# Kernel optimization log

Measured on AMD Instinct MI355X. Metric: run time of the kernel, lower is better.

## Reference

```python
import jax, jax.numpy as jnp
import numpy as np

PI = np.pi


def _rot(axis, a):
    c, s = jnp.cos(a), jnp.sin(a)
    o, z = jnp.ones_like(a), jnp.zeros_like(a)
    if axis == 'X':
        flat = (o, z, z, z, c, -s, z, s, c)
    elif axis == 'Y':
        flat = (c, z, s, z, o, z, -s, z, c)
    else:  # 'Z'
        flat = (c, -s, z, s, c, z, z, z, o)
    return jnp.stack(flat, -1).reshape(3, 3)


def setup_inputs() -> dict:
    key = jax.random.key(0)
    k1, k2 = jax.random.split(key)
    H, W = 1080, 1920
    # world points: spread ~50 around origin, camera at z=100 looking back
    PntCld = jax.random.normal(k1, (400000, 3), dtype=jnp.float32) * 50.0
    # detected corners in pixel coordinates
    dtcCor = jax.random.uniform(k2, (128, 2), dtype=jnp.float32) * jnp.array([W, H], jnp.float32)
    cam_pos = jnp.array([0.0, 0.0, 100.0], jnp.float32)
    theta = jnp.array([5.0, -3.0, 10.0], jnp.float32)  # degrees
    view_angle = jnp.array([60.0], jnp.float32)        # degrees
    return {"PntCld": PntCld, "dtcCor": dtcCor, "cam_pos": cam_pos,
            "theta": theta, "view_angle": view_angle, "height": H, "width": W}


def reference(PntCld, dtcCor, cam_pos, theta, view_angle, height, width):
    th = theta * (PI / 180.0)
    R = _rot('Z', th[2]) @ (_rot('Y', th[1]) @ _rot('X', th[0]))  # (3,3)
    f = -height / (2.0 * jnp.tan(view_angle[0] / 2.0 * (PI / 180.0)))
    K = jnp.stack([f, 0.0, width / 2 - 0.5,
                   0.0, f, height / 2 - 0.5,
                   0.0, 0.0, 1.0]).reshape(3, 3)
    translated = PntCld - cam_pos                 # (N_p,3)
    xyz = translated @ R.T                        # rotate each point
    xyz_prime = xyz / xyz[:, 2:3]                 # perspective divide
    uv = xyz_prime @ K.T                          # (N_p,3) pixel coords
    # y-invert and shift by image height, keep (u,v)
    uv_final = jnp.stack([uv[:, 0], height - uv[:, 1]], -1)  # (N_p,2)
    # pairwise squared distances via ||a||^2 + ||b||^2 - 2 a.b (no (N_d,N_p,2) tensor)
    d2 = (jnp.sum(dtcCor ** 2, -1)[:, None]
          + jnp.sum(uv_final ** 2, -1)[None, :]
          - 2.0 * dtcCor @ uv_final.T)            # (N_d,N_p)
    return jnp.sum(jnp.min(d2, axis=1))
```

## Files before the change

kernel.cpp:

```cpp
#include <hip/hip_runtime.h>
#include <math.h>

#define TILE  512
#define BLOCK 256
#define NC    128


__global__ void init_kernel(const float* __restrict__ theta,
                            const float* __restrict__ vang,
                            const int* __restrict__ hh,
                            const int* __restrict__ ww,
                            float* __restrict__ scal,
                            float* __restrict__ out) {
    if (threadIdx.x == 0) {
        const double D2R = 0.017453292519943295;
        double a = (double)theta[0] * D2R;
        double b = (double)theta[1] * D2R;
        double c = (double)theta[2] * D2R;
        double sa = sin(a), ca = cos(a);
        double sb = sin(b), cb = cos(b);
        double sc = sin(c), cc = cos(c);
        double H = (double)hh[0], W = (double)ww[0];
        double fd = -H / (2.0 * tan((double)vang[0] * 0.5 * D2R));
        scal[0] = (float)(cc * cb);
        scal[1] = (float)(cc * sb * sa - sc * ca);
        scal[2] = (float)(cc * sb * ca + sc * sa);
        scal[3] = (float)(sc * cb);
        scal[4] = (float)(sc * sb * sa + cc * ca);
        scal[5] = (float)(sc * sb * ca - cc * sa);
        scal[6] = (float)(-sb);
        scal[7] = (float)(cb * sa);
        scal[8] = (float)(cb * ca);
        scal[9]  = (float)fd;
        scal[10] = (float)(W * 0.5 - 0.5);
        scal[11] = (float)(H * 0.5 + 0.5);
        out[0] = 0.0f;
    }
}

__global__ __launch_bounds__(BLOCK) void proj_min_kernel(
        const float* __restrict__ pnt,
        const float* __restrict__ cor,
        const float* __restrict__ cam,
        const float* __restrict__ scal,
        float* __restrict__ pbmin,
        int n, int NB) {
    __shared__ float4 uvb[TILE];
    __shared__ float red[4 * NC];

    const int tid = threadIdx.x;
    const float r00 = scal[0], r01 = scal[1], r02 = scal[2];
    const float r10 = scal[3], r11 = scal[4], r12 = scal[5];
    const float r20 = scal[6], r21 = scal[7], r22 = scal[8];
    const float f = scal[9], cx = scal[10], cyv = scal[11];
    const float c0 = cam[0], c1 = cam[1], c2 = cam[2];

    const int base = blockIdx.x * TILE;

    #pragma unroll
    for (int k = 0; k < TILE; k += BLOCK) {
        int i = base + k + tid;
        float u = 0.f, vf = 0.f, b2 = 3.0e38f;
        if (i < n) {
            float px = pnt[3 * i], py = pnt[3 * i + 1], pz = pnt[3 * i + 2];
            float tx = px - c0, ty = py - c1, tz = pz - c2;
            float x = fmaf(r00, tx, fmaf(r01, ty, r02 * tz));
            float y = fmaf(r10, tx, fmaf(r11, ty, r12 * tz));
            float z = fmaf(r20, tx, fmaf(r21, ty, r22 * tz));
            float xz = x / z, yz = y / z;
            u  = fmaf(f, xz, cx);
            vf = fmaf(-f, yz, cyv);
            b2 = fmaf(u, u, vf * vf);
        }
        uvb[k + tid] = make_float4(u, vf, b2, 0.f);
    }
    __syncthreads();

    const int lane = tid & 63;
    const int w    = tid >> 6;
    const int h    = lane >> 5;
    const int sl   = lane & 31;
    const int cb   = sl << 2;

    float bx[4], by[4], m[4];
    #pragma unroll
    for (int k = 0; k < 4; ++k) {
        bx[k] = -2.f * cor[2 * (cb + k)];
        by[k] = -2.f * cor[2 * (cb + k) + 1];
        m[k]  = 3.4e38f;
    }

    const float4* p = &uvb[(w << 7) + (h << 6)];
    #pragma unroll 8
    for (int j = 0; j < 64; ++j) {
        float4 q = p[j];
        #pragma unroll
        for (int k = 0; k < 4; ++k)
            m[k] = fminf(m[k], fmaf(bx[k], q.x, fmaf(by[k], q.y, q.z)));
    }

    #pragma unroll
    for (int k = 0; k < 4; ++k)
        m[k] = fminf(m[k], __shfl_xor(m[k], 32));
    if (lane < 32) {
        #pragma unroll
        for (int k = 0; k < 4; ++k)
            red[w * NC + cb + k] = m[k];
    }
    __syncthreads();

    if (tid < NC) {
        float mm = fminf(fminf(red[tid], red[NC + tid]),
                         fminf(red[2 * NC + tid], red[3 * NC + tid]));
        pbmin[tid * NB + blockIdx.x] = mm;
    }
}

__global__ void reduce_kernel(const float* __restrict__ pbmin,
                              const float* __restrict__ cor,
                              float* __restrict__ out, int NB) {
    const int c = blockIdx.x;
    const int t = threadIdx.x;
    const float* row = pbmin + c * NB;
    float m = 3.4e38f;
    for (int i = t; i < NB; i += 64) m = fminf(m, row[i]);
    #pragma unroll
    for (int off = 32; off > 0; off >>= 1)
        m = fminf(m, __shfl_down(m, off));
    if (t == 0) {
        float ax = cor[2 * c], ay = cor[2 * c + 1];
        atomicAdd(out, m + fmaf(ax, ax, ay * ay));
    }
}

extern "C" void kernel_launch(void* const* d_in, const int* in_sizes, int n_in,
                              void* d_out, int out_size, void* d_ws, size_t ws_size,
                              hipStream_t stream) {
    const float* pnt   = (const float*)d_in[0];
    const float* cor   = (const float*)d_in[1];
    const float* cam   = (const float*)d_in[2];
    const float* theta = (const float*)d_in[3];
    const float* vang  = (const float*)d_in[4];
    const int*   hh    = (const int*)d_in[5];
    const int*   ww    = (const int*)d_in[6];

    int n  = in_sizes[0] / 3;
    int NB = (n + TILE - 1) / TILE;

    float* scal  = (float*)d_ws;
    float* pbmin = (float*)((char*)d_ws + 256);

    init_kernel<<<1, 64, 0, stream>>>(theta, vang, hh, ww, scal, (float*)d_out);
    proj_min_kernel<<<NB, BLOCK, 0, stream>>>(pnt, cor, cam, scal, pbmin, n, NB);
    reduce_kernel<<<NC, 64, 0, stream>>>(pbmin, cor, (float*)d_out, NB);
}
```

Measured before the change: 80.52 us.

## Fold init into projection kernel, vectorize point loads, transpose partial-min layout

The separate init kernel is removed. Each block now computes the rotation and intrinsics scalars in thread 0 and shares them through LDS, which trades one launch for redundant per-block double-precision trig. Each thread loads two consecutive points with three float2 loads instead of strided scalar loads. The partial-min buffer is stored block-major so the column reduction reads coalesced-ish across blocks. The atomicAdd is replaced by a staged deterministic double-precision sum kernel, which adds one extra small launch.

```diff
diff --git a/kernel.cpp b/kernel.cpp
--- a/kernel.cpp
+++ b/kernel.cpp
@@ -6,73 +6,92 @@
 #define NC    128
 
 
-__global__ void init_kernel(const float* __restrict__ theta,
-                            const float* __restrict__ vang,
-                            const int* __restrict__ hh,
-                            const int* __restrict__ ww,
-                            float* __restrict__ scal,
-                            float* __restrict__ out) {
-    if (threadIdx.x == 0) {
+__global__ __launch_bounds__(BLOCK) void proj_min_kernel(
+        const float* __restrict__ pnt,
+        const float* __restrict__ cor,
+        const float* __restrict__ cam,
+        const float* __restrict__ theta,
+        const float* __restrict__ vang,
+        const int* __restrict__ hh,
+        const int* __restrict__ ww,
+        float* __restrict__ pbmin,
+        int n) {
+    __shared__ float4 uvb[TILE];
+    __shared__ float red[4 * NC];
+    __shared__ float sc[12];
+
+    const int tid  = threadIdx.x;
+    const int base = blockIdx.x * TILE;
+
+    const int i0 = base + 2 * tid;
+    float p0x = 0.f, p0y = 0.f, p0z = 0.f;
+    float p1x = 0.f, p1y = 0.f, p1z = 0.f;
+    const bool v0 = (i0 < n), v1 = (i0 + 1 < n);
+    if (v1) {
+        const float2* q = (const float2*)(pnt + 3 * i0);
+        float2 a = q[0], b = q[1], c = q[2];
+        p0x = a.x; p0y = a.y; p0z = b.x;
+        p1x = b.y; p1y = c.x; p1z = c.y;
+    } else if (v0) {
+        p0x = pnt[3 * i0]; p0y = pnt[3 * i0 + 1]; p0z = pnt[3 * i0 + 2];
+    }
+
+    if (tid == 0) {
         const double D2R = 0.017453292519943295;
         double a = (double)theta[0] * D2R;
         double b = (double)theta[1] * D2R;
         double c = (double)theta[2] * D2R;
         double sa = sin(a), ca = cos(a);
         double sb = sin(b), cb = cos(b);
-        double sc = sin(c), cc = cos(c);
+        double sc_ = sin(c), cc = cos(c);
         double H = (double)hh[0], W = (double)ww[0];
         double fd = -H / (2.0 * tan((double)vang[0] * 0.5 * D2R));
-        scal[0] = (float)(cc * cb);
-        scal[1] = (float)(cc * sb * sa - sc * ca);
-        scal[2] = (float)(cc * sb * ca + sc * sa);
-        scal[3] = (float)(sc * cb);
-        scal[4] = (float)(sc * sb * sa + cc * ca);
-        scal[5] = (float)(sc * sb * ca - cc * sa);
-        scal[6] = (float)(-sb);
-        scal[7] = (float)(cb * sa);
-        scal[8] = (float)(cb * ca);
-        scal[9]  = (float)fd;
-        scal[10] = (float)(W * 0.5 - 0.5);
-        scal[11] = (float)(H * 0.5 + 0.5);
-        out[0] = 0.0f;
+        sc[0] = (float)(cc * cb);
+        sc[1] = (float)(cc * sb * sa - sc_ * ca);
+        sc[2] = (float)(cc * sb * ca + sc_ * sa);
+        sc[3] = (float)(sc_ * cb);
+        sc[4] = (float)(sc_ * sb * sa + cc * ca);
+        sc[5] = (float)(sc_ * sb * ca - cc * sa);
+        sc[6] = (float)(-sb);
+        sc[7] = (float)(cb * sa);
+        sc[8] = (float)(cb * ca);
+        sc[9]  = (float)fd;
+        sc[10] = (float)(W * 0.5 - 0.5);
+        sc[11] = (float)(H * 0.5 + 0.5);
     }
-}
+    __syncthreads();
 
-__global__ __launch_bounds__(BLOCK) void proj_min_kernel(
-        const float* __restrict__ pnt,
-        const float* __restrict__ cor,
-        const float* __restrict__ cam,
-        const float* __restrict__ scal,
-        float* __restrict__ pbmin,
-        int n, int NB) {
-    __shared__ float4 uvb[TILE];
-    __shared__ float red[4 * NC];
-
-    const int tid = threadIdx.x;
-    const float r00 = scal[0], r01 = scal[1], r02 = scal[2];
-    const float r10 = scal[3], r11 = scal[4], r12 = scal[5];
-    const float r20 = scal[6], r21 = scal[7], r22 = scal[8];
-    const float f = scal[9], cx = scal[10], cyv = scal[11];
+    const float r00 = sc[0], r01 = sc[1], r02 = sc[2];
+    const float r10 = sc[3], r11 = sc[4], r12 = sc[5];
+    const float r20 = sc[6], r21 = sc[7], r22 = sc[8];
+    const float f = sc[9], cx = sc[10], cyv = sc[11];
     const float c0 = cam[0], c1 = cam[1], c2 = cam[2];
 
-    const int base = blockIdx.x * TILE;
-
-    #pragma unroll
-    for (int k = 0; k < TILE; k += BLOCK) {
-        int i = base + k + tid;
-        float u = 0.f, vf = 0.f, b2 = 3.0e38f;
-        if (i < n) {
-            float px = pnt[3 * i], py = pnt[3 * i + 1], pz = pnt[3 * i + 2];
-            float tx = px - c0, ty = py - c1, tz = pz - c2;
+    {
+        float u0 = 0.f, w0 = 0.f, b20 = 3.0e38f;
+        float u1 = 0.f, w1 = 0.f, b21 = 3.0e38f;
+        if (v0) {
+            float tx = p0x - c0, ty = p0y - c1, tz = p0z - c2;
             float x = fmaf(r00, tx, fmaf(r01, ty, r02 * tz));
             float y = fmaf(r10, tx, fmaf(r11, ty, r12 * tz));
             float z = fmaf(r20, tx, fmaf(r21, ty, r22 * tz));
             float xz = x / z, yz = y / z;
-            u  = fmaf(f, xz, cx);
-            vf = fmaf(-f, yz, cyv);
-            b2 = fmaf(u, u, vf * vf);
+            u0 = fmaf(f, xz, cx);
+            w0 = fmaf(-f, yz, cyv);
+            b20 = fmaf(u0, u0, w0 * w0);
         }
-        uvb[k + tid] = make_float4(u, vf, b2, 0.f);
+        if (v1) {
+            float tx = p1x - c0, ty = p1y - c1, tz = p1z - c2;
+            float x = fmaf(r00, tx, fmaf(r01, ty, r02 * tz));
+            float y = fmaf(r10, tx, fmaf(r11, ty, r12 * tz));
+            float z = fmaf(r20, tx, fmaf(r21, ty, r22 * tz));
+            float xz = x / z, yz = y / z;
+            u1 = fmaf(f, xz, cx);
+            w1 = fmaf(-f, yz, cyv);
+            b21 = fmaf(u1, u1, w1 * w1);
+        }
+        uvb[2 * tid]     = make_float4(u0, w0, b20, 0.f);
+        uvb[2 * tid + 1] = make_float4(u1, w1, b21, 0.f);
     }
     __syncthreads();
 
@@ -112,25 +131,36 @@
     if (tid < NC) {
         float mm = fminf(fminf(red[tid], red[NC + tid]),
                          fminf(red[2 * NC + tid], red[3 * NC + tid]));
-        pbmin[tid * NB + blockIdx.x] = mm;
+        pbmin[blockIdx.x * NC + tid] = mm;
     }
 }
 
-__global__ void reduce_kernel(const float* __restrict__ pbmin,
-                              const float* __restrict__ cor,
-                              float* __restrict__ out, int NB) {
+__global__ __launch_bounds__(64) void colmin_kernel(
+        const float* __restrict__ pbmin,
+        const float* __restrict__ cor,
+        float* __restrict__ stage, int NB) {
     const int c = blockIdx.x;
     const int t = threadIdx.x;
-    const float* row = pbmin + c * NB;
     float m = 3.4e38f;
-    for (int i = t; i < NB; i += 64) m = fminf(m, row[i]);
+    for (int r = t; r < NB; r += 64)
+        m = fminf(m, pbmin[r * NC + c]);
     #pragma unroll
     for (int off = 32; off > 0; off >>= 1)
         m = fminf(m, __shfl_down(m, off));
     if (t == 0) {
         float ax = cor[2 * c], ay = cor[2 * c + 1];
-        atomicAdd(out, m + fmaf(ax, ax, ay * ay));
+        stage[c] = m + fmaf(ax, ax, ay * ay);
     }
+}
+
+__global__ void sum_kernel(const float* __restrict__ stage,
+                           float* __restrict__ out) {
+    const int t = threadIdx.x;
+    double s = (double)stage[t] + (double)stage[t + 64];
+    #pragma unroll
+    for (int off = 32; off > 0; off >>= 1)
+        s += __shfl_down(s, off);
+    if (t == 0) out[0] = (float)s;
 }
 
 extern "C" void kernel_launch(void* const* d_in, const int* in_sizes, int n_in,
@@ -147,10 +177,11 @@
     int n  = in_sizes[0] / 3;
     int NB = (n + TILE - 1) / TILE;
 
-    float* scal  = (float*)d_ws;
-    float* pbmin = (float*)((char*)d_ws + 256);
+    float* pbmin = (float*)d_ws;
+    float* stage = (float*)((char*)d_ws + 448 * 1024);
 
-    init_kernel<<<1, 64, 0, stream>>>(theta, vang, hh, ww, scal, (float*)d_out);
-    proj_min_kernel<<<NB, BLOCK, 0, stream>>>(pnt, cor, cam, scal, pbmin, n, NB);
-    reduce_kernel<<<NC, 64, 0, stream>>>(pbmin, cor, (float*)d_out, NB);
+    proj_min_kernel<<<NB, BLOCK, 0, stream>>>(pnt, cor, cam, theta, vang,
+                                              hh, ww, pbmin, n);
+    colmin_kernel<<<NC, 64, 0, stream>>>(pbmin, cor, stage, NB);
+    sum_kernel<<<1, 64, 0, stream>>>(stage, (float*)d_out);
 }
```

Result: no change. 79.72 us (-1.0%).
